# Performance work log

Hardware: AMD Instinct MI355X
Metric: run time of the kernel (lower is better)

## Reference

```python
import jax, jax.numpy as jnp
import numpy as np

TOP_K = 2

def setup_inputs() -> dict:
    key = jax.random.key(0)
    k1, k2 = jax.random.split(key)
    B, S, D, E = 4, 8192, 1024, 64
    hidden_states = jax.random.normal(k1, (B, S, D), dtype=jnp.float32)
    gate_weight = jax.random.normal(k2, (E, D), dtype=jnp.float32) * (1.0 / D ** 0.5)
    return {"hidden_states": hidden_states, "gate_weight": gate_weight}

def reference(hidden_states, gate_weight):
    # router_logits: [B, S, E] = hidden @ W^T
    router_logits = jnp.einsum('bsd,ed->bse', hidden_states, gate_weight)
    # softmax in float32 (matches .float() in torch), cast back to input dtype
    router_probs = jax.nn.softmax(router_logits.astype(jnp.float32), axis=-1).astype(hidden_states.dtype)
    top_k_probs, selected_experts = jax.lax.top_k(router_probs, TOP_K)
    top_k_probs = top_k_probs / (jnp.sum(top_k_probs, axis=-1, keepdims=True) + 1e-08)
    return top_k_probs, selected_experts, router_logits
```

## Files before the change

### kernel.cpp

```cpp
#include <hip/hip_runtime.h>
#include <math.h>


typedef __attribute__((ext_vector_type(8))) short bf16x8;
typedef __attribute__((ext_vector_type(4))) float f32x4;

static constexpr int TOKENS = 32768;
static constexpr int DDIM   = 1024;
static constexpr int NEXP   = 64;
static constexpr size_t OFF_EXP = 65536;
static constexpr size_t OFF_LOG = 131072;

__global__ void w_split3_kernel(const float* __restrict__ w,
                                short* __restrict__ w1,
                                short* __restrict__ w2,
                                short* __restrict__ w3) {
    int idx = blockIdx.x * blockDim.x + threadIdx.x;
    for (int i = idx; i < NEXP * DDIM; i += gridDim.x * blockDim.x) {
        int e = i >> 10, k = i & 1023;
        float f = w[i];
        unsigned u1 = __float_as_uint(f);
        float f1 = __uint_as_float(u1 & 0xffff0000u);
        float r1 = f - f1;
        unsigned u2 = __float_as_uint(r1);
        float f2 = __uint_as_float(u2 & 0xffff0000u);
        float r2 = r1 - f2;
        unsigned u3 = __float_as_uint(r2);
        int n = e >> 4, c = k >> 5;
        int lane = (e & 15) + ((k & 31) >> 3) * 16;
        int j = k & 7;
        size_t dst = ((size_t)(c * 4 + n) * 64 + lane) * 8 + j;
        w1[dst] = (short)(u1 >> 16);
        w2[dst] = (short)(u2 >> 16);
        w3[dst] = (short)(u3 >> 16);
    }
}

__device__ inline void split8(float4 a, float4 b,
                              bf16x8& o1, bf16x8& o2, bf16x8& o3) {
    float f[8] = {a.x, a.y, a.z, a.w, b.x, b.y, b.z, b.w};
#pragma unroll
    for (int j = 0; j < 8; ++j) {
        unsigned u1 = __float_as_uint(f[j]);
        float f1 = __uint_as_float(u1 & 0xffff0000u);
        float r1 = f[j] - f1;
        unsigned u2 = __float_as_uint(r1);
        float f2 = __uint_as_float(u2 & 0xffff0000u);
        float r2 = r1 - f2;
        o1[j] = (short)(u1 >> 16);
        o2[j] = (short)(u2 >> 16);
        o3[j] = (short)(__float_as_uint(r2) >> 16);
    }
}

typedef const __attribute__((address_space(1))) unsigned int* gas1_t;
typedef __attribute__((address_space(3))) unsigned int* las3_t;
__device__ inline void stage16(const void* g, void* l) {
    __builtin_amdgcn_global_load_lds((gas1_t)(uintptr_t)g,
                                     (las3_t)(uintptr_t)l, 16, 0, 0);
}

__global__ __launch_bounds__(512, 4)
void router_mfma_kernel(const float* __restrict__ h,
                        const short* __restrict__ w1,
                        const short* __restrict__ w2,
                        const short* __restrict__ w3,
                        float* __restrict__ out) {
    __shared__ alignas(16) char smem[49152];
    const int tid   = threadIdx.x;
    const int lane  = tid & 63;
    const int wv    = tid >> 6;
    const int khalf = wv & 1;
    const int mg    = wv >> 1;
    const int token0 = blockIdx.x * 64 + mg * 16;
    const int arow  = lane & 15;
    const int ks    = lane >> 4;

    const float* ap = h + (size_t)(token0 + arow) * DDIM + khalf * 512 + ks * 8;

    const short* warr[3] = {w1, w2, w3};
    const char* gsrc[3];
    int ldso[3];
#pragma unroll
    for (int i = 0; i < 3; ++i) {
        int seg = wv * 3 + i;
        int kh = seg & 1;
        int an = seg >> 1;
        int a = an >> 2, n = an & 3;
        gsrc[i] = (const char*)warr[a] + (size_t)(kh * 64 + n) * 1024 + lane * 16;
        ldso[i] = (kh * 12 + a * 4 + n) * 1024;
    }

#define STAGE(bb, cc)                                                      \
    {                                                                      \
        _Pragma("unroll")                                                  \
        for (int i = 0; i < 3; ++i)                                        \
            stage16(gsrc[i] + (size_t)(cc) * 4096,                         \
                    smem + (bb) * 24576 + ldso[i]);                        \
    }

    f32x4 acc[4];
#pragma unroll
    for (int n = 0; n < 4; ++n)
#pragma unroll
        for (int r = 0; r < 4; ++r) acc[n][r] = 0.0f;

    float4 a0c = *reinterpret_cast<const float4*>(ap);
    float4 a1c = *reinterpret_cast<const float4*>(ap + 4);
    STAGE(0, 0);
    __syncthreads();

    float4 a0n, a1n;
#pragma unroll 2
    for (int t = 0; t < 16; ++t) {
        const int b = t & 1;
        if (t < 15) {
            STAGE(b ^ 1, t + 1);
            a0n = *reinterpret_cast<const float4*>(ap + (t + 1) * 32);
            a1n = *reinterpret_cast<const float4*>(ap + (t + 1) * 32 + 4);
        }

        bf16x8 A1f, A2f, A3f;
        split8(a0c, a1c, A1f, A2f, A3f);

        const char* wb = smem + b * 24576 + khalf * 12288 + lane * 16;
#pragma unroll
        for (int n = 0; n < 4; ++n) {
            bf16x8 W1v = *reinterpret_cast<const bf16x8*>(wb + n * 1024);
            bf16x8 W2v = *reinterpret_cast<const bf16x8*>(wb + n * 1024 + 4096);
            bf16x8 W3v = *reinterpret_cast<const bf16x8*>(wb + n * 1024 + 8192);
            f32x4 t2 = acc[n];
            t2 = __builtin_amdgcn_mfma_f32_16x16x32_bf16(A3f, W1v, t2, 0, 0, 0);
            t2 = __builtin_amdgcn_mfma_f32_16x16x32_bf16(A1f, W3v, t2, 0, 0, 0);
            t2 = __builtin_amdgcn_mfma_f32_16x16x32_bf16(A2f, W2v, t2, 0, 0, 0);
            t2 = __builtin_amdgcn_mfma_f32_16x16x32_bf16(A2f, W1v, t2, 0, 0, 0);
            t2 = __builtin_amdgcn_mfma_f32_16x16x32_bf16(A1f, W2v, t2, 0, 0, 0);
            t2 = __builtin_amdgcn_mfma_f32_16x16x32_bf16(A1f, W1v, t2, 0, 0, 0);
            acc[n] = t2;
        }
        __syncthreads();
        a0c = a0n; a1c = a1n;
    }

    if (khalf == 1) {
        float* c = (float*)smem + (size_t)(mg * 64 + lane) * 17;
#pragma unroll
        for (int n = 0; n < 4; ++n)
#pragma unroll
            for (int r = 0; r < 4; ++r) c[n * 4 + r] = acc[n][r];
    }
    __syncthreads();
    if (khalf != 0) return;

    {
        const float* c = (const float*)smem + (size_t)(mg * 64 + lane) * 17;
#pragma unroll
        for (int n = 0; n < 4; ++n)
#pragma unroll
            for (int r = 0; r < 4; ++r) acc[n][r] += c[n * 4 + r];
    }

    const int rbase = (lane >> 4) * 4;
    const int col   = lane & 15;

#pragma unroll
    for (int n = 0; n < 4; ++n)
#pragma unroll
        for (int r = 0; r < 4; ++r)
            out[OFF_LOG + (size_t)(token0 + rbase + r) * NEXP + n * 16 + col]
                = acc[n][r];

#pragma unroll
    for (int r = 0; r < 4; ++r) {
        const int token = token0 + rbase + r;
        float mx = fmaxf(fmaxf(acc[0][r], acc[1][r]),
                         fmaxf(acc[2][r], acc[3][r]));
#pragma unroll
        for (int d = 1; d <= 8; d <<= 1) mx = fmaxf(mx, __shfl_xor(mx, d, 64));

        float p[4];
        float s = 0.0f;
#pragma unroll
        for (int n = 0; n < 4; ++n) { p[n] = expf(acc[n][r] - mx); s += p[n]; }
#pragma unroll
        for (int d = 1; d <= 8; d <<= 1) s += __shfl_xor(s, d, 64);

        float v1 = -INFINITY, v2 = -INFINITY;
        int   i1 = NEXP,      i2 = NEXP;
#pragma unroll
        for (int n = 0; n < 4; ++n) {
            float v = p[n];
            int   ei = n * 16 + col;
            if (v > v1)      { v2 = v1; i2 = i1; v1 = v; i1 = ei; }
            else if (v > v2) { v2 = v;  i2 = ei; }
        }

#pragma unroll
        for (int d = 1; d <= 8; d <<= 1) {
            float ov1 = __shfl_xor(v1, d, 64);
            float ov2 = __shfl_xor(v2, d, 64);
            int   oi1 = __shfl_xor(i1, d, 64);
            int   oi2 = __shfl_xor(i2, d, 64);
            bool ofirst = (ov1 > v1) || (ov1 == v1 && oi1 < i1);
            float n1, n2; int ni1, ni2;
            if (ofirst) {
                n1 = ov1; ni1 = oi1;
                bool sec = (v1 > ov2) || (v1 == ov2 && i1 < oi2);
                n2 = sec ? v1 : ov2; ni2 = sec ? i1 : oi2;
            } else {
                n1 = v1; ni1 = i1;
                bool sec = (ov1 > v2) || (ov1 == v2 && oi1 < i2);
                n2 = sec ? ov1 : v2; ni2 = sec ? oi1 : i2;
            }
            v1 = n1; i1 = ni1; v2 = n2; i2 = ni2;
        }

        if (col == 0) {
            float t1 = v1 / s;
            float t2 = v2 / s;
            float dn = t1 + t2 + 1e-8f;
            float2 pr; pr.x = t1 / dn; pr.y = t2 / dn;
            *reinterpret_cast<float2*>(out + (size_t)token * 2) = pr;
            float2 ex; ex.x = (float)i1; ex.y = (float)i2;
            *reinterpret_cast<float2*>(out + OFF_EXP + (size_t)token * 2) = ex;
        }
    }
#undef STAGE
}

extern "C" void kernel_launch(void* const* d_in, const int* in_sizes, int n_in,
                              void* d_out, int out_size, void* d_ws, size_t ws_size,
                              hipStream_t stream) {
    const float* h = (const float*)d_in[0];
    const float* w = (const float*)d_in[1];
    float* out = (float*)d_out;
    short* w1 = (short*)d_ws;
    short* w2 = w1 + (size_t)NEXP * DDIM;
    short* w3 = w2 + (size_t)NEXP * DDIM;
    hipLaunchKernelGGL(w_split3_kernel, dim3(128), dim3(256), 0, stream, w, w1, w2, w3);
    hipLaunchKernelGGL(router_mfma_kernel, dim3(TOKENS / 64), dim3(512), 0, stream,
                       h, w1, w2, w3, out);
}
```

Before: 43.64 us.

## Prefetch activations two iterations ahead with register ring and manual waitcnt barriers

Result: no change. 44.50 us (+2.0%).

```diff
diff --git a/kernel.cpp b/kernel.cpp
--- a/kernel.cpp
+++ b/kernel.cpp
@@ -105,23 +105,29 @@
 #pragma unroll
         for (int r = 0; r < 4; ++r) acc[n][r] = 0.0f;
 
-    float4 a0c = *reinterpret_cast<const float4*>(ap);
-    float4 a1c = *reinterpret_cast<const float4*>(ap + 4);
+    float4 ring[3][2];
+
     STAGE(0, 0);
-    __syncthreads();
-
-    float4 a0n, a1n;
-#pragma unroll 2
+    ring[0][0] = *reinterpret_cast<const float4*>(ap);
+    ring[0][1] = *reinterpret_cast<const float4*>(ap + 4);
+    ring[1][0] = *reinterpret_cast<const float4*>(ap + 32);
+    ring[1][1] = *reinterpret_cast<const float4*>(ap + 36);
+    asm volatile("s_waitcnt vmcnt(4)" ::: "memory");
+    __builtin_amdgcn_s_barrier();
+
+#pragma unroll
     for (int t = 0; t < 16; ++t) {
         const int b = t & 1;
-        if (t < 15) {
-            STAGE(b ^ 1, t + 1);
-            a0n = *reinterpret_cast<const float4*>(ap + (t + 1) * 32);
-            a1n = *reinterpret_cast<const float4*>(ap + (t + 1) * 32 + 4);
+        if (t < 15) STAGE(b ^ 1, t + 1);
+        if (t < 14) {
+            ring[(t + 2) % 3][0] =
+                *reinterpret_cast<const float4*>(ap + (t + 2) * 32);
+            ring[(t + 2) % 3][1] =
+                *reinterpret_cast<const float4*>(ap + (t + 2) * 32 + 4);
         }
 
         bf16x8 A1f, A2f, A3f;
-        split8(a0c, a1c, A1f, A2f, A3f);
+        split8(ring[t % 3][0], ring[t % 3][1], A1f, A2f, A3f);
 
         const char* wb = smem + b * 24576 + khalf * 12288 + lane * 16;
 #pragma unroll
@@ -138,8 +144,14 @@
             t2 = __builtin_amdgcn_mfma_f32_16x16x32_bf16(A1f, W1v, t2, 0, 0, 0);
             acc[n] = t2;
         }
-        __syncthreads();
-        a0c = a0n; a1c = a1n;
+
+        if (t < 14) {
+            asm volatile("s_waitcnt vmcnt(2)" ::: "memory");
+            __builtin_amdgcn_s_barrier();
+        } else if (t == 14) {
+            asm volatile("s_waitcnt vmcnt(0)" ::: "memory");
+            __builtin_amdgcn_s_barrier();
+        }
     }
 
     if (khalf == 1) {
```

## Give each wave full K range for 16 tokens, doubling tokens per block

Applied to the files above, without the earlier changes.

Result: slower. 47.09 us (+7.9%).

```diff
diff --git a/kernel.cpp b/kernel.cpp
--- a/kernel.cpp
+++ b/kernel.cpp
@@ -70,13 +70,11 @@
     const int tid   = threadIdx.x;
     const int lane  = tid & 63;
     const int wv    = tid >> 6;
-    const int khalf = wv & 1;
-    const int mg    = wv >> 1;
-    const int token0 = blockIdx.x * 64 + mg * 16;
+    const int token0 = blockIdx.x * 128 + wv * 16;
     const int arow  = lane & 15;
     const int ks    = lane >> 4;
 
-    const float* ap = h + (size_t)(token0 + arow) * DDIM + khalf * 512 + ks * 8;
+    const float* ap = h + (size_t)(token0 + arow) * DDIM + ks * 8;
 
     const short* warr[3] = {w1, w2, w3};
     const char* gsrc[3];
@@ -84,81 +82,95 @@
 #pragma unroll
     for (int i = 0; i < 3; ++i) {
         int seg = wv * 3 + i;
-        int kh = seg & 1;
-        int an = seg >> 1;
-        int a = an >> 2, n = an & 3;
-        gsrc[i] = (const char*)warr[a] + (size_t)(kh * 64 + n) * 1024 + lane * 16;
-        ldso[i] = (kh * 12 + a * 4 + n) * 1024;
-    }
-
-#define STAGE(bb, cc)                                                      \
+        int kc = seg / 12;
+        int rem = seg % 12;
+        int a = rem >> 2, n = rem & 3;
+        gsrc[i] = (const char*)warr[a] + (size_t)kc * 65536 + n * 1024 + lane * 16;
+        ldso[i] = (kc * 12 + a * 4 + n) * 1024;
+    }
+
+#define STAGE(bb, tt)                                                      \
     {                                                                      \
         _Pragma("unroll")                                                  \
         for (int i = 0; i < 3; ++i)                                        \
-            stage16(gsrc[i] + (size_t)(cc) * 4096,                         \
+            stage16(gsrc[i] + (size_t)(tt) * 4096,                         \
                     smem + (bb) * 24576 + ldso[i]);                        \
     }
 
-    f32x4 acc[4];
+    f32x4 accA[4], accB[4];
 #pragma unroll
     for (int n = 0; n < 4; ++n)
 #pragma unroll
-        for (int r = 0; r < 4; ++r) acc[n][r] = 0.0f;
-
-    float4 a0c = *reinterpret_cast<const float4*>(ap);
-    float4 a1c = *reinterpret_cast<const float4*>(ap + 4);
+        for (int r = 0; r < 4; ++r) { accA[n][r] = 0.0f; accB[n][r] = 0.0f; }
+
+    float4 ring[2][2][2];
+
     STAGE(0, 0);
-    __syncthreads();
-
-    float4 a0n, a1n;
-#pragma unroll 2
+    ring[0][0][0] = *reinterpret_cast<const float4*>(ap);
+    ring[0][0][1] = *reinterpret_cast<const float4*>(ap + 4);
+    ring[0][1][0] = *reinterpret_cast<const float4*>(ap + 512);
+    ring[0][1][1] = *reinterpret_cast<const float4*>(ap + 516);
+    asm volatile("s_waitcnt vmcnt(4)" ::: "memory");
+    __builtin_amdgcn_s_barrier();
+
+#pragma unroll
     for (int t = 0; t < 16; ++t) {
         const int b = t & 1;
-        if (t < 15) {
+        if (t + 1 < 16) {
             STAGE(b ^ 1, t + 1);
-            a0n = *reinterpret_cast<const float4*>(ap + (t + 1) * 32);
-            a1n = *reinterpret_cast<const float4*>(ap + (t + 1) * 32 + 4);
-        }
-
-        bf16x8 A1f, A2f, A3f;
-        split8(a0c, a1c, A1f, A2f, A3f);
-
-        const char* wb = smem + b * 24576 + khalf * 12288 + lane * 16;
+            ring[b ^ 1][0][0] =
+                *reinterpret_cast<const float4*>(ap + (t + 1) * 32);
+            ring[b ^ 1][0][1] =
+                *reinterpret_cast<const float4*>(ap + (t + 1) * 32 + 4);
+            ring[b ^ 1][1][0] =
+                *reinterpret_cast<const float4*>(ap + 512 + (t + 1) * 32);
+            ring[b ^ 1][1][1] =
+                *reinterpret_cast<const float4*>(ap + 512 + (t + 1) * 32 + 4);
+        }
+
+        bf16x8 A1a, A2a, A3a, A1b, A2b, A3b;
+        split8(ring[b][0][0], ring[b][0][1], A1a, A2a, A3a);
+        split8(ring[b][1][0], ring[b][1][1], A1b, A2b, A3b);
+
+        const char* wb0 = smem + b * 24576 + lane * 16;
+        const char* wb1 = wb0 + 12288;
 #pragma unroll
         for (int n = 0; n < 4; ++n) {
-            bf16x8 W1v = *reinterpret_cast<const bf16x8*>(wb + n * 1024);
-            bf16x8 W2v = *reinterpret_cast<const bf16x8*>(wb + n * 1024 + 4096);
-            bf16x8 W3v = *reinterpret_cast<const bf16x8*>(wb + n * 1024 + 8192);
-            f32x4 t2 = acc[n];
-            t2 = __builtin_amdgcn_mfma_f32_16x16x32_bf16(A3f, W1v, t2, 0, 0, 0);
-            t2 = __builtin_amdgcn_mfma_f32_16x16x32_bf16(A1f, W3v, t2, 0, 0, 0);
-            t2 = __builtin_amdgcn_mfma_f32_16x16x32_bf16(A2f, W2v, t2, 0, 0, 0);
-            t2 = __builtin_amdgcn_mfma_f32_16x16x32_bf16(A2f, W1v, t2, 0, 0, 0);
-            t2 = __builtin_amdgcn_mfma_f32_16x16x32_bf16(A1f, W2v, t2, 0, 0, 0);
-            t2 = __builtin_amdgcn_mfma_f32_16x16x32_bf16(A1f, W1v, t2, 0, 0, 0);
-            acc[n] = t2;
-        }
-        __syncthreads();
-        a0c = a0n; a1c = a1n;
-    }
-
-    if (khalf == 1) {
-        float* c = (float*)smem + (size_t)(mg * 64 + lane) * 17;
-#pragma unroll
-        for (int n = 0; n < 4; ++n)
-#pragma unroll
-            for (int r = 0; r < 4; ++r) c[n * 4 + r] = acc[n][r];
-    }
-    __syncthreads();
-    if (khalf != 0) return;
-
-    {
-        const float* c = (const float*)smem + (size_t)(mg * 64 + lane) * 17;
-#pragma unroll
-        for (int n = 0; n < 4; ++n)
-#pragma unroll
-            for (int r = 0; r < 4; ++r) acc[n][r] += c[n * 4 + r];
-    }
+            bf16x8 W1v = *reinterpret_cast<const bf16x8*>(wb0 + n * 1024);
+            bf16x8 W2v = *reinterpret_cast<const bf16x8*>(wb0 + n * 1024 + 4096);
+            bf16x8 W3v = *reinterpret_cast<const bf16x8*>(wb0 + n * 1024 + 8192);
+            f32x4 t0 = accA[n];
+            t0 = __builtin_amdgcn_mfma_f32_16x16x32_bf16(A3a, W1v, t0, 0, 0, 0);
+            t0 = __builtin_amdgcn_mfma_f32_16x16x32_bf16(A1a, W3v, t0, 0, 0, 0);
+            t0 = __builtin_amdgcn_mfma_f32_16x16x32_bf16(A2a, W2v, t0, 0, 0, 0);
+            t0 = __builtin_amdgcn_mfma_f32_16x16x32_bf16(A2a, W1v, t0, 0, 0, 0);
+            t0 = __builtin_amdgcn_mfma_f32_16x16x32_bf16(A1a, W2v, t0, 0, 0, 0);
+            t0 = __builtin_amdgcn_mfma_f32_16x16x32_bf16(A1a, W1v, t0, 0, 0, 0);
+            accA[n] = t0;
+            bf16x8 X1v = *reinterpret_cast<const bf16x8*>(wb1 + n * 1024);
+            bf16x8 X2v = *reinterpret_cast<const bf16x8*>(wb1 + n * 1024 + 4096);
+            bf16x8 X3v = *reinterpret_cast<const bf16x8*>(wb1 + n * 1024 + 8192);
+            f32x4 t1 = accB[n];
+            t1 = __builtin_amdgcn_mfma_f32_16x16x32_bf16(A3b, X1v, t1, 0, 0, 0);
+            t1 = __builtin_amdgcn_mfma_f32_16x16x32_bf16(A1b, X3v, t1, 0, 0, 0);
+            t1 = __builtin_amdgcn_mfma_f32_16x16x32_bf16(A2b, X2v, t1, 0, 0, 0);
+            t1 = __builtin_amdgcn_mfma_f32_16x16x32_bf16(A2b, X1v, t1, 0, 0, 0);
+            t1 = __builtin_amdgcn_mfma_f32_16x16x32_bf16(A1b, X2v, t1, 0, 0, 0);
+            t1 = __builtin_amdgcn_mfma_f32_16x16x32_bf16(A1b, X1v, t1, 0, 0, 0);
+            accB[n] = t1;
+        }
+
+        if (t + 1 < 16) {
+            asm volatile("s_waitcnt vmcnt(4)" ::: "memory");
+            __builtin_amdgcn_s_barrier();
+        }
+    }
+
+    f32x4 acc[4];
+#pragma unroll
+    for (int n = 0; n < 4; ++n)
+#pragma unroll
+        for (int r = 0; r < 4; ++r) acc[n][r] = accA[n][r] + accB[n][r];
 
     const int rbase = (lane >> 4) * 4;
     const int col   = lane & 15;
@@ -238,6 +250,6 @@
     short* w2 = w1 + (size_t)NEXP * DDIM;
     short* w3 = w2 + (size_t)NEXP * DDIM;
     hipLaunchKernelGGL(w_split3_kernel, dim3(128), dim3(256), 0, stream, w, w1, w2, w3);
-    hipLaunchKernelGGL(router_mfma_kernel, dim3(TOKENS / 64), dim3(512), 0, stream,
+    hipLaunchKernelGGL(router_mfma_kernel, dim3(TOKENS / 128), dim3(512), 0, stream,
                        h, w1, w2, w3, out);
 }
```
